# Optimization experiments

Measured on AMD Instinct MI355X. Metric: run time of the kernel, lower is better.

## Reference

```python
import jax, jax.numpy as jnp
import numpy as np

N = 100000   # nodes
E = 1600000  # edges (avg degree 16)
HID = 128    # in_feats = n_hidden
P = 100000   # pos/neg link pairs
L = 3        # GIN layers
BN_EPS = 1e-5


def setup_inputs() -> dict:
    key = jax.random.key(0)
    ks = jax.random.split(key, 16)
    s = 1.0 / np.sqrt(HID)  # ~ torch linear init scale
    inp = {
        "x": jax.random.normal(ks[0], (N, HID), jnp.float32),
        "src": jax.random.randint(ks[1], (E,), 0, N, jnp.int32),
        "dst": jax.random.randint(ks[2], (E,), 0, N, jnp.int32),
        "pos_src": jax.random.randint(ks[3], (P,), 0, N, jnp.int32),
        "pos_dst": jax.random.randint(ks[4], (P,), 0, N, jnp.int32),
        "neg_src": jax.random.randint(ks[5], (P,), 0, N, jnp.int32),
        "neg_dst": jax.random.randint(ks[6], (P,), 0, N, jnp.int32),
        "W0": jax.random.normal(ks[7], (L, HID, HID), jnp.float32) * s,
        "W1": jax.random.normal(ks[8], (L, HID, HID), jnp.float32) * s,
        "g_mlp": jnp.ones((L, HID), jnp.float32),
        "b_mlp": jnp.zeros((L, HID), jnp.float32),
        "g_apply": jnp.ones((L, HID), jnp.float32),
        "b_apply": jnp.zeros((L, HID), jnp.float32),
        "g_out": jnp.ones((L - 1, HID), jnp.float32),
        "b_out": jnp.zeros((L - 1, HID), jnp.float32),
        "pW1": jax.random.normal(ks[9], (HID, HID), jnp.float32) * s,
        "pb1": jnp.zeros((HID,), jnp.float32),
        "pW2": jax.random.normal(ks[10], (HID, HID), jnp.float32) * s,
        "pb2": jnp.zeros((HID,), jnp.float32),
        "pW3": jax.random.normal(ks[11], (1, HID), jnp.float32) * s,
        "pb3": jnp.zeros((1,), jnp.float32),
    }
    return inp


def _bn(h, g, b):
    # training-mode BatchNorm1d: batch stats, biased variance
    mu = jnp.mean(h, axis=0)
    var = jnp.mean(jnp.square(h - mu), axis=0)
    return g * (h - mu) * jax.lax.rsqrt(var + BN_EPS) + b


def reference(x, src, dst, pos_src, pos_dst, neg_src, neg_dst,
              W0, W1, g_mlp, b_mlp, g_apply, b_apply, g_out, b_out,
              pW1, pb1, pW2, pb2, pW3, pb3):
    # in-degree for mean aggregation (clamped to avoid div-by-zero)
    deg = jnp.maximum(
        jax.ops.segment_sum(jnp.ones((E,), x.dtype), dst, num_segments=N), 1.0)
    h = x
    for l in range(L):
        # GINConv, eps = 0: h_dst + mean over in-neighbors
        agg = jax.ops.segment_sum(h[src], dst, num_segments=N) / deg[:, None]
        z = h + agg
        # ApplyNodeFunc: MLP(2 layers, no bias) with inner BN+ReLU, then BN+ReLU
        m = jax.nn.relu(_bn(z @ W0[l].T, g_mlp[l], b_mlp[l]))
        m = m @ W1[l].T
        h = jax.nn.relu(_bn(m, g_apply[l], b_apply[l]))
        if l < L - 1:
            # outer BN + ReLU (dropout is identity in eval)
            h = jax.nn.relu(_bn(h, g_out[l], b_out[l]))

    def predict(hs, hd):
        t = hs * hd
        t = jax.nn.relu(t @ pW1.T + pb1)
        t = jax.nn.relu(t @ pW2.T + pb2)
        return t @ pW3.T + pb3  # [P, 1]

    h_pos = predict(h[pos_src], h[pos_dst])
    h_neg = predict(h[neg_src], h[neg_dst])
    return (h_pos, h_neg)
```

## Files before the change

kernel.cpp:

```cpp
#include <hip/hip_runtime.h>

#define HID 128
#define BN_EPS 1e-5f

typedef __bf16 bf16;
typedef __attribute__((ext_vector_type(8))) __bf16 bf16x8;
typedef __attribute__((ext_vector_type(4))) float f32x4;

__device__ __forceinline__ float bnrelu(float x, float a, float c) {
  return fmaxf(fmaf(a, x, c), 0.f);
}

__global__ void hist_k(const int* __restrict__ dst, int* __restrict__ cnt, int E) {
  int i = blockIdx.x * blockDim.x + threadIdx.x;
  if (i < E) atomicAdd(&cnt[dst[i]], 1);
}

__global__ __launch_bounds__(256)
void scan1_k(const int* __restrict__ cnt, int* __restrict__ bsum, int Nn) {
  __shared__ int red[4];
  int tid = threadIdx.x;
  int base = blockIdx.x * 1024;
  int s = 0;
#pragma unroll
  for (int u = 0; u < 4; ++u) {
    int i = base + u * 256 + tid;
    if (i < Nn) s += cnt[i];
  }
#pragma unroll
  for (int d = 1; d < 64; d <<= 1) s += __shfl_xor(s, d, 64);
  int lane = tid & 63, wv = tid >> 6;
  if (lane == 0) red[wv] = s;
  __syncthreads();
  if (tid == 0) bsum[blockIdx.x] = red[0] + red[1] + red[2] + red[3];
}

__global__ void scan2_k(int* __restrict__ bsum, int G) {
  int lane = threadIdx.x;
  int carry = 0;
  for (int base = 0; base < G; base += 64) {
    int i = base + lane;
    int v = (i < G) ? bsum[i] : 0;
    int x = v;
#pragma unroll
    for (int d = 1; d < 64; d <<= 1) { int t = __shfl_up(x, d, 64); if (lane >= d) x += t; }
    if (i < G) bsum[i] = carry + x - v;
    carry += __shfl(x, 63, 64);
  }
}

__global__ __launch_bounds__(256)
void scan3_k(const int* __restrict__ cnt, const int* __restrict__ boff,
             int* __restrict__ row_start, int Nn, int E) {
  __shared__ int wtot[4];
  int tid = threadIdx.x, lane = tid & 63, wv = tid >> 6;
  int i0 = blockIdx.x * 1024 + tid * 4;
  int t0 = 0, t1 = 0, t2 = 0, t3 = 0;
  if (i0 + 3 < Nn) {
    int4 v = *(const int4*)(cnt + i0);
    t0 = v.x; t1 = v.y; t2 = v.z; t3 = v.w;
  } else {
    if (i0     < Nn) t0 = cnt[i0];
    if (i0 + 1 < Nn) t1 = cnt[i0 + 1];
    if (i0 + 2 < Nn) t2 = cnt[i0 + 2];
    if (i0 + 3 < Nn) t3 = cnt[i0 + 3];
  }
  int tsum = t0 + t1 + t2 + t3;
  int x = tsum;
#pragma unroll
  for (int d = 1; d < 64; d <<= 1) { int t = __shfl_up(x, d, 64); if (lane >= d) x += t; }
  if (lane == 63) wtot[wv] = x;
  __syncthreads();
  int wo = 0;
  for (int k = 0; k < wv; ++k) wo += wtot[k];
  int base = boff[blockIdx.x] + wo + x - tsum;
  if (i0     < Nn) row_start[i0] = base;
  if (i0 + 1 < Nn) row_start[i0 + 1] = base + t0;
  if (i0 + 2 < Nn) row_start[i0 + 2] = base + t0 + t1;
  if (i0 + 3 < Nn) row_start[i0 + 3] = base + t0 + t1 + t2;
  if (blockIdx.x == 0 && tid == 0) row_start[Nn] = E;
}

__global__ void init64_k(const int* __restrict__ row_start, int* __restrict__ bcur64,
                         int Nn, int NB2) {
  int i = threadIdx.x;
  if (i < NB2) {
    int n = i << 11; if (n > Nn) n = Nn;
    bcur64[i] = row_start[n];
  }
}

__global__ __launch_bounds__(256)
void part64_k(const int* __restrict__ src, const int* __restrict__ dst,
              int* __restrict__ bcur64, unsigned* __restrict__ ebuf2, int E) {
  __shared__ int lcnt[64], gbase[64], lcur[64];
  int tid = threadIdx.x;
  if (tid < 64) { lcnt[tid] = 0; lcur[tid] = 0; }
  __syncthreads();
  int base = blockIdx.x * 2048;
  int ok[8]; unsigned pk[8]; int bk[8];
#pragma unroll
  for (int u = 0; u < 8; ++u) {
    int e = base + u * 256 + tid;
    if (e < E) {
      int s = src[e], d = dst[e];
      ok[u] = 1; bk[u] = d >> 11;
      pk[u] = ((unsigned)(d & 2047) << 17) | (unsigned)s;
      atomicAdd(&lcnt[bk[u]], 1);
    } else ok[u] = 0;
  }
  __syncthreads();
  if (tid < 64 && lcnt[tid]) gbase[tid] = atomicAdd(&bcur64[tid], lcnt[tid]);
  __syncthreads();
#pragma unroll
  for (int u = 0; u < 8; ++u) if (ok[u]) {
    int sl = atomicAdd(&lcur[bk[u]], 1);
    ebuf2[gbase[bk[u]] + sl] = pk[u];
  }
}

__global__ __launch_bounds__(1024)
void fill2_k(const unsigned* __restrict__ ebuf2, const int* __restrict__ row_start,
             int* __restrict__ csr, int Nn) {
  __shared__ int ncur[2048];
  int tid = threadIdx.x;
  ncur[tid] = 0; ncur[tid + 1024] = 0;
  __syncthreads();
  int nb0 = blockIdx.x << 11;
  int hi = nb0 + 2048; if (hi > Nn) hi = Nn;
  int beg = row_start[nb0], end = row_start[hi];
  for (int e = beg + tid; e < end; e += 1024) {
    unsigned v = ebuf2[e];
    int dl = v >> 17, s = (int)(v & 0x1FFFF);
    int p = atomicAdd(&ncur[dl], 1);
    csr[row_start[nb0 + dl] + p] = s;
  }
}

__global__ __launch_bounds__(256)
void wconv_k(const float* __restrict__ W0, const float* __restrict__ W1,
             const float* __restrict__ pW1, const float* __restrict__ pW2,
             bf16* __restrict__ Wb) {
  int idx = (blockIdx.x * 256 + threadIdx.x) * 4;
  int seg = idx >> 14, loc = idx & 16383;
  const float* srcp = seg < 3 ? W0 + (size_t)seg * 16384
                    : seg < 6 ? W1 + (size_t)(seg - 3) * 16384
                    : seg == 6 ? pW1 : pW2;
  float4 v = *(const float4*)(srcp + loc);
  union { bf16 h[4]; unsigned long long u; } pk;
  pk.h[0] = (bf16)v.x; pk.h[1] = (bf16)v.y; pk.h[2] = (bf16)v.z; pk.h[3] = (bf16)v.w;
  *(unsigned long long*)(Wb + idx) = pk.u;
}

template<int MODE>
__global__ __launch_bounds__(256)
void agg_k(const float* __restrict__ H,
           const float* __restrict__ ac1, const float* __restrict__ g1, const float* __restrict__ b1,
           const float* __restrict__ ac2, const float* __restrict__ g2, const float* __restrict__ b2,
           float invN,
           const int* __restrict__ row_start, const int* __restrict__ csr,
           bf16* __restrict__ Z, int Nn) {
  __shared__ float sA2[128], sC2[128], sA3[128], sC3[128];
  int tid = threadIdx.x;
  if (MODE) {
    if (tid < 128) {
      float mu = ac1[tid] * invN;
      float var = fmaxf(ac1[128 + tid] * invN - mu * mu, 0.f);
      float a = g1[tid] * rsqrtf(var + BN_EPS);
      sA2[tid] = a; sC2[tid] = fmaf(-a, mu, b1[tid]);
      mu = ac2[tid] * invN;
      var = fmaxf(ac2[128 + tid] * invN - mu * mu, 0.f);
      a = g2[tid] * rsqrtf(var + BN_EPS);
      sA3[tid] = a; sC3[tid] = fmaf(-a, mu, b2[tid]);
    }
    __syncthreads();
  }
  int wv = tid >> 6, lane = tid & 63;
  int n = blockIdx.x * 4 + wv;
  if (n >= Nn) return;
  int c0 = lane * 2;
  float A2x = 0, A2y = 0, C2x = 0, C2y = 0, A3x = 0, A3y = 0, C3x = 0, C3y = 0;
  if (MODE) {
    A2x = sA2[c0]; A2y = sA2[c0 + 1]; C2x = sC2[c0]; C2y = sC2[c0 + 1];
    A3x = sA3[c0]; A3y = sA3[c0 + 1]; C3x = sC3[c0]; C3y = sC3[c0 + 1];
  }
  int beg = row_start[n], end = row_start[n + 1];
  float2 hn = *(const float2*)(H + (size_t)n * HID + c0);
  float inv = 1.f / fmaxf((float)(end - beg), 1.f);
  float ax0 = 0, ay0 = 0, ax1 = 0, ay1 = 0, ax2 = 0, ay2 = 0, ax3 = 0, ay3 = 0;
  int j = beg;
  for (; j + 8 <= end; j += 8) {
    int s0 = csr[j], s1 = csr[j + 1], s2 = csr[j + 2], s3 = csr[j + 3];
    int s4 = csr[j + 4], s5 = csr[j + 5], s6 = csr[j + 6], s7 = csr[j + 7];
    float2 v0 = *(const float2*)(H + (size_t)s0 * HID + c0);
    float2 v1 = *(const float2*)(H + (size_t)s1 * HID + c0);
    float2 v2 = *(const float2*)(H + (size_t)s2 * HID + c0);
    float2 v3 = *(const float2*)(H + (size_t)s3 * HID + c0);
    float2 v4 = *(const float2*)(H + (size_t)s4 * HID + c0);
    float2 v5 = *(const float2*)(H + (size_t)s5 * HID + c0);
    float2 v6 = *(const float2*)(H + (size_t)s6 * HID + c0);
    float2 v7 = *(const float2*)(H + (size_t)s7 * HID + c0);
    if (MODE) {
      v0.x = bnrelu(bnrelu(v0.x, A2x, C2x), A3x, C3x); v0.y = bnrelu(bnrelu(v0.y, A2y, C2y), A3y, C3y);
      v1.x = bnrelu(bnrelu(v1.x, A2x, C2x), A3x, C3x); v1.y = bnrelu(bnrelu(v1.y, A2y, C2y), A3y, C3y);
      v2.x = bnrelu(bnrelu(v2.x, A2x, C2x), A3x, C3x); v2.y = bnrelu(bnrelu(v2.y, A2y, C2y), A3y, C3y);
      v3.x = bnrelu(bnrelu(v3.x, A2x, C2x), A3x, C3x); v3.y = bnrelu(bnrelu(v3.y, A2y, C2y), A3y, C3y);
      v4.x = bnrelu(bnrelu(v4.x, A2x, C2x), A3x, C3x); v4.y = bnrelu(bnrelu(v4.y, A2y, C2y), A3y, C3y);
      v5.x = bnrelu(bnrelu(v5.x, A2x, C2x), A3x, C3x); v5.y = bnrelu(bnrelu(v5.y, A2y, C2y), A3y, C3y);
      v6.x = bnrelu(bnrelu(v6.x, A2x, C2x), A3x, C3x); v6.y = bnrelu(bnrelu(v6.y, A2y, C2y), A3y, C3y);
      v7.x = bnrelu(bnrelu(v7.x, A2x, C2x), A3x, C3x); v7.y = bnrelu(bnrelu(v7.y, A2y, C2y), A3y, C3y);
    }
    ax0 += v0.x; ay0 += v0.y; ax1 += v1.x; ay1 += v1.y;
    ax2 += v2.x; ay2 += v2.y; ax3 += v3.x; ay3 += v3.y;
    ax0 += v4.x; ay0 += v4.y; ax1 += v5.x; ay1 += v5.y;
    ax2 += v6.x; ay2 += v6.y; ax3 += v7.x; ay3 += v7.y;
  }
  for (; j < end; ++j) {
    int s = csr[j];
    float2 v = *(const float2*)(H + (size_t)s * HID + c0);
    if (MODE) {
      v.x = bnrelu(bnrelu(v.x, A2x, C2x), A3x, C3x);
      v.y = bnrelu(bnrelu(v.y, A2y, C2y), A3y, C3y);
    }
    ax0 += v.x; ay0 += v.y;
  }
  float ax = (ax0 + ax1) + (ax2 + ax3);
  float ay = (ay0 + ay1) + (ay2 + ay3);
  float hx = hn.x, hy = hn.y;
  if (MODE) {
    hx = bnrelu(bnrelu(hx, A2x, C2x), A3x, C3x);
    hy = bnrelu(bnrelu(hy, A2y, C2y), A3y, C3y);
  }
  float zx = hx + ax * inv, zy = hy + ay * inv;
  union { bf16 h[2]; unsigned u; } pk;
  pk.h[0] = (bf16)zx; pk.h[1] = (bf16)zy;
  *(unsigned*)((char*)Z + ((size_t)n * HID + c0) * 2) = pk.u;
}

template<int AMODE>
__global__ __launch_bounds__(256)
void gemm_k(const void* __restrict__ Asrc,
            const float* __restrict__ acIn, const float* __restrict__ g, const float* __restrict__ b,
            float invN,
            const bf16* __restrict__ Wb, float* __restrict__ C,
            float* __restrict__ accumOut, int Nrows) {
  __shared__ float sA[128], sC[128], sSum[128], sSq[128];
  int tid = threadIdx.x;
  if (tid < 128) {
    sSum[tid] = 0.f; sSq[tid] = 0.f;
    if (AMODE) {
      float mu = acIn[tid] * invN;
      float var = fmaxf(acIn[128 + tid] * invN - mu * mu, 0.f);
      float a = g[tid] * rsqrtf(var + BN_EPS);
      sA[tid] = a; sC[tid] = fmaf(-a, mu, b[tid]);
    }
  }
  __syncthreads();
  int wv = tid >> 6, lane = tid & 63;
  int lm = lane & 15, lg = lane >> 4;
  int rowbase = blockIdx.x * 128 + wv * 32;
  f32x4 acc[2][8] = {};
#pragma unroll
  for (int kk = 0; kk < 4; ++kk) {
    int kb = kk * 32 + lg * 8;
    bf16x8 af[2];
    if (AMODE == 0) {
      const bf16* Zp = (const bf16*)Asrc;
#pragma unroll
      for (int rt = 0; rt < 2; ++rt) {
        int row = rowbase + rt * 16 + lm; if (row > Nrows - 1) row = Nrows - 1;
        af[rt] = *(const bf16x8*)(Zp + (size_t)row * HID + kb);
      }
    } else {
      const float* Tp = (const float*)Asrc;
      float4 a0 = *(const float4*)(sA + kb), a1 = *(const float4*)(sA + kb + 4);
      float4 q0 = *(const float4*)(sC + kb), q1 = *(const float4*)(sC + kb + 4);
#pragma unroll
      for (int rt = 0; rt < 2; ++rt) {
        int row = rowbase + rt * 16 + lm; if (row > Nrows - 1) row = Nrows - 1;
        const float* p = Tp + (size_t)row * HID + kb;
        float4 x0 = *(const float4*)p, x1 = *(const float4*)(p + 4);
        bf16x8 f;
        f[0] = (bf16)bnrelu(x0.x, a0.x, q0.x); f[1] = (bf16)bnrelu(x0.y, a0.y, q0.y);
        f[2] = (bf16)bnrelu(x0.z, a0.z, q0.z); f[3] = (bf16)bnrelu(x0.w, a0.w, q0.w);
        f[4] = (bf16)bnrelu(x1.x, a1.x, q1.x); f[5] = (bf16)bnrelu(x1.y, a1.y, q1.y);
        f[6] = (bf16)bnrelu(x1.z, a1.z, q1.z); f[7] = (bf16)bnrelu(x1.w, a1.w, q1.w);
        af[rt] = f;
      }
    }
    bf16x8 bfr[8];
#pragma unroll
    for (int ct = 0; ct < 8; ++ct)
      bfr[ct] = *(const bf16x8*)(Wb + (size_t)(ct * 16 + lm) * HID + kb);
#pragma unroll
    for (int rt = 0; rt < 2; ++rt)
#pragma unroll
      for (int ct = 0; ct < 8; ++ct)
        acc[rt][ct] = __builtin_amdgcn_mfma_f32_16x16x32_bf16(af[rt], bfr[ct], acc[rt][ct], 0, 0, 0);
  }
#pragma unroll
  for (int ct = 0; ct < 8; ++ct) {
    int col = ct * 16 + lm;
    float ps = 0.f, pq = 0.f;
#pragma unroll
    for (int rt = 0; rt < 2; ++rt) {
#pragma unroll
      for (int i = 0; i < 4; ++i) {
        int row = rowbase + rt * 16 + lg * 4 + i;
        if (row < Nrows) {
          float v = acc[rt][ct][i];
          C[(size_t)row * HID + col] = v;
          ps += v; pq = fmaf(v, v, pq);
        }
      }
    }
    ps += __shfl_xor(ps, 16, 64); ps += __shfl_xor(ps, 32, 64);
    pq += __shfl_xor(pq, 16, 64); pq += __shfl_xor(pq, 32, 64);
    if (lane < 16) { atomicAdd(&sSum[col], ps); atomicAdd(&sSq[col], pq); }
  }
  __syncthreads();
  if (tid < 128) {
    atomicAdd(&accumOut[tid], sSum[tid]);
    atomicAdd(&accumOut[128 + tid], sSq[tid]);
  }
}

__global__ __launch_bounds__(256)
void stats1_k(const float* __restrict__ T, const float* __restrict__ acIn,
              const float* __restrict__ g, const float* __restrict__ b, float invN,
              float* __restrict__ accumOut, int Nrows) {
  int col = threadIdx.x & 127, half = threadIdx.x >> 7;
  float mu = acIn[col] * invN;
  float var = fmaxf(acIn[128 + col] * invN - mu * mu, 0.f);
  float av = g[col] * rsqrtf(var + BN_EPS);
  float cv = fmaf(-av, mu, b[col]);
  float s = 0.f, sq = 0.f;
  for (int r = blockIdx.x * 2 + half; r < Nrows; r += gridDim.x * 2) {
    float x = T[(size_t)r * HID + col];
    x = fmaxf(fmaf(av, x, cv), 0.f);
    s += x; sq = fmaf(x, x, sq);
  }
  __shared__ float sb[256], qb[256];
  sb[threadIdx.x] = s; qb[threadIdx.x] = sq;
  __syncthreads();
  if (half == 0) {
    s += sb[threadIdx.x + 128]; sq += qb[threadIdx.x + 128];
    atomicAdd(&accumOut[col], s); atomicAdd(&accumOut[128 + col], sq);
  }
}

__global__ __launch_bounds__(256)
void pred_k(const float* __restrict__ T, const float* __restrict__ acIn,
            const float* __restrict__ g, const float* __restrict__ b, float invN,
            const int* __restrict__ ps, const int* __restrict__ pd,
            const int* __restrict__ ns, const int* __restrict__ nd,
            const bf16* __restrict__ W1b, const float* __restrict__ b1p,
            const bf16* __restrict__ W2b, const float* __restrict__ b2p,
            const float* __restrict__ w3, const float* __restrict__ b3,
            float* __restrict__ out, int Pn) {
  __shared__ bf16 At[128 * 128];
  __shared__ float sAp[128], sCp[128];
  int tid = threadIdx.x;
  if (tid < 128) {
    float mu = acIn[tid] * invN;
    float var = fmaxf(acIn[128 + tid] * invN - mu * mu, 0.f);
    float a = g[tid] * rsqrtf(var + BN_EPS);
    sAp[tid] = a; sCp[tid] = fmaf(-a, mu, b[tid]);
  }
  __syncthreads();
  int q0 = blockIdx.x * 128;
  {
    int r = tid >> 1;
    int q = q0 + r;
    int cb = (tid & 1) * 64;
    if (q < 2 * Pn) {
      int s, d;
      if (q < Pn) { s = ps[q]; d = pd[q]; } else { s = ns[q - Pn]; d = nd[q - Pn]; }
      const float* rs_ = T + (size_t)s * HID;
      const float* rd_ = T + (size_t)d * HID;
      for (int c = cb; c < cb + 64; c += 4) {
        float4 xs = *(const float4*)(rs_ + c);
        float4 xd = *(const float4*)(rd_ + c);
        float4 av = *(const float4*)(sAp + c);
        float4 cv = *(const float4*)(sCp + c);
        float t0 = bnrelu(xs.x, av.x, cv.x) * bnrelu(xd.x, av.x, cv.x);
        float t1 = bnrelu(xs.y, av.y, cv.y) * bnrelu(xd.y, av.y, cv.y);
        float t2 = bnrelu(xs.z, av.z, cv.z) * bnrelu(xd.z, av.z, cv.z);
        float t3 = bnrelu(xs.w, av.w, cv.w) * bnrelu(xd.w, av.w, cv.w);
        union { bf16 h[4]; unsigned long long u; } pk;
        pk.h[0] = (bf16)t0; pk.h[1] = (bf16)t1; pk.h[2] = (bf16)t2; pk.h[3] = (bf16)t3;
        unsigned addr = (unsigned)(r * 256 + c * 2);
        addr ^= (unsigned)((r & 7) << 4);
        *(unsigned long long*)((char*)At + addr) = pk.u;
      }
    } else {
      for (int c = cb; c < cb + 64; c += 4) {
        unsigned addr = (unsigned)(r * 256 + c * 2);
        addr ^= (unsigned)((r & 7) << 4);
        *(unsigned long long*)((char*)At + addr) = 0ull;
      }
    }
  }
  __syncthreads();
  int wv = tid >> 6, lane = tid & 63;
  int lm = lane & 15, lg = lane >> 4;
  const f32x4 vzero = {0.f, 0.f, 0.f, 0.f};
  f32x4 acc[2][8];
#pragma unroll
  for (int r = 0; r < 2; ++r) for (int c = 0; c < 8; ++c) acc[r][c] = vzero;
#pragma unroll
  for (int kk = 0; kk < 4; ++kk) {
    bf16x8 af[2];
#pragma unroll
    for (int rt = 0; rt < 2; ++rt) {
      int row = wv * 32 + rt * 16 + lm;
      unsigned addr = (unsigned)(row * 256 + kk * 64 + lg * 16);
      addr ^= (unsigned)((row & 7) << 4);
      af[rt] = *(const bf16x8*)((char*)At + addr);
    }
    bf16x8 bfr[8];
#pragma unroll
    for (int ct = 0; ct < 8; ++ct)
      bfr[ct] = *(const bf16x8*)(W1b + (size_t)(ct * 16 + lm) * HID + kk * 32 + lg * 8);
#pragma unroll
    for (int rt = 0; rt < 2; ++rt)
#pragma unroll
      for (int ct = 0; ct < 8; ++ct)
        acc[rt][ct] = __builtin_amdgcn_mfma_f32_16x16x32_bf16(af[rt], bfr[ct], acc[rt][ct], 0, 0, 0);
  }
  __syncthreads();
#pragma unroll
  for (int rt = 0; rt < 2; ++rt)
#pragma unroll
    for (int ct = 0; ct < 8; ++ct) {
      int col = ct * 16 + lm;
      float bb = b1p[col];
#pragma unroll
      for (int i = 0; i < 4; ++i) {
        int row = wv * 32 + rt * 16 + lg * 4 + i;
        float v = fmaxf(acc[rt][ct][i] + bb, 0.f);
        unsigned addr = (unsigned)(row * 256 + col * 2);
        addr ^= (unsigned)((row & 7) << 4);
        *(bf16*)((char*)At + addr) = (bf16)v;
      }
    }
  __syncthreads();
#pragma unroll
  for (int r = 0; r < 2; ++r) for (int c = 0; c < 8; ++c) acc[r][c] = vzero;
#pragma unroll
  for (int kk = 0; kk < 4; ++kk) {
    bf16x8 af[2];
#pragma unroll
    for (int rt = 0; rt < 2; ++rt) {
      int row = wv * 32 + rt * 16 + lm;
      unsigned addr = (unsigned)(row * 256 + kk * 64 + lg * 16);
      addr ^= (unsigned)((row & 7) << 4);
      af[rt] = *(const bf16x8*)((char*)At + addr);
    }
    bf16x8 bfr[8];
#pragma unroll
    for (int ct = 0; ct < 8; ++ct)
      bfr[ct] = *(const bf16x8*)(W2b + (size_t)(ct * 16 + lm) * HID + kk * 32 + lg * 8);
#pragma unroll
    for (int rt = 0; rt < 2; ++rt)
#pragma unroll
      for (int ct = 0; ct < 8; ++ct)
        acc[rt][ct] = __builtin_amdgcn_mfma_f32_16x16x32_bf16(af[rt], bfr[ct], acc[rt][ct], 0, 0, 0);
  }
  float b2v[8], w3v[8];
#pragma unroll
  for (int ct = 0; ct < 8; ++ct) { b2v[ct] = b2p[ct * 16 + lm]; w3v[ct] = w3[ct * 16 + lm]; }
  float b3s = b3[0];
#pragma unroll
  for (int rt = 0; rt < 2; ++rt) {
#pragma unroll
    for (int i = 0; i < 4; ++i) {
      float p = 0.f;
#pragma unroll
      for (int ct = 0; ct < 8; ++ct)
        p += fmaxf(acc[rt][ct][i] + b2v[ct], 0.f) * w3v[ct];
      p += __shfl_xor(p, 1); p += __shfl_xor(p, 2);
      p += __shfl_xor(p, 4); p += __shfl_xor(p, 8);
      int row = wv * 32 + rt * 16 + lg * 4 + i;
      int q = q0 + row;
      if (lm == 0 && q < 2 * Pn) out[q] = p + b3s;
    }
  }
}

extern "C" void kernel_launch(void* const* d_in, const int* in_sizes, int n_in,
                              void* d_out, int out_size, void* d_ws, size_t ws_size,
                              hipStream_t stream) {
  const float* x  = (const float*)d_in[0];
  const int* src  = (const int*)d_in[1];
  const int* dst  = (const int*)d_in[2];
  const int* ps   = (const int*)d_in[3];
  const int* pd   = (const int*)d_in[4];
  const int* ns   = (const int*)d_in[5];
  const int* nd   = (const int*)d_in[6];
  const float* W0 = (const float*)d_in[7];
  const float* W1 = (const float*)d_in[8];
  const float* g_mlp   = (const float*)d_in[9];
  const float* b_mlp   = (const float*)d_in[10];
  const float* g_apply = (const float*)d_in[11];
  const float* b_apply = (const float*)d_in[12];
  const float* g_out   = (const float*)d_in[13];
  const float* b_out   = (const float*)d_in[14];
  const float* pW1 = (const float*)d_in[15];
  const float* pb1 = (const float*)d_in[16];
  const float* pW2 = (const float*)d_in[17];
  const float* pb2 = (const float*)d_in[18];
  const float* pW3 = (const float*)d_in[19];
  const float* pb3 = (const float*)d_in[20];
  float* out = (float*)d_out;

  const int N = in_sizes[0] / HID;
  const int E = in_sizes[1];
  const int P = in_sizes[3];
  const int NB2 = (N + 2047) >> 11;

  char* w = (char*)d_ws;
  size_t off = 0;
  auto alloc = [&](size_t bytes) -> void* {
    void* p = w + off;
    off = (off + bytes + 255) & ~(size_t)255;
    return p;
  };
  bf16*  Z   = (bf16*)alloc((size_t)N * HID * 2);
  float* TA  = (float*)alloc((size_t)N * HID * 4);
  float* TB  = (float*)alloc((size_t)N * HID * 4);
  int*   csr = (int*)alloc((size_t)E * 4);
  unsigned* ebuf2 = (unsigned*)alloc((size_t)E * 4);
  int*   row_start = (int*)alloc((size_t)(N + 1) * 4);
  size_t zoff = off;
  int*   cnt   = (int*)alloc((size_t)N * 4);
  float* accum = (float*)alloc(9 * 256 * 4);
  size_t zbytes = off - zoff;
  int*   bsum   = (int*)alloc(256 * 4);
  int*   bcur64 = (int*)alloc(64 * 4);
  bf16*  Wb = (bf16*)alloc(8 * 16384 * 2);
  (void)ws_size; (void)n_in; (void)out_size;

  const int G = (N + 1023) / 1024;
  const float invN = 1.f / (float)N;

  hipMemsetAsync(w + zoff, 0, zbytes, stream);
  int gridE = (E + 255) / 256;
  hist_k<<<gridE, 256, 0, stream>>>(dst, cnt, E);
  scan1_k<<<G, 256, 0, stream>>>(cnt, bsum, N);
  scan2_k<<<1, 64, 0, stream>>>(bsum, G);
  scan3_k<<<G, 256, 0, stream>>>(cnt, bsum, row_start, N, E);
  init64_k<<<1, 64, 0, stream>>>(row_start, bcur64, N, NB2);
  part64_k<<<(E + 2047) / 2048, 256, 0, stream>>>(src, dst, bcur64, ebuf2, E);
  fill2_k<<<NB2, 1024, 0, stream>>>(ebuf2, row_start, csr, N);
  wconv_k<<<128, 256, 0, stream>>>(W0, W1, pW1, pW2, Wb);

  int gridN4 = (N + 3) / 4;
  int gridG  = (N + 127) / 128;

  for (int l = 0; l < 3; ++l) {
    int s0 = l * 3 + 0, s1 = l * 3 + 1, s2 = l * 3 + 2;
    if (l == 0)
      agg_k<0><<<gridN4, 256, 0, stream>>>(x, nullptr, nullptr, nullptr,
                                           nullptr, nullptr, nullptr, invN,
                                           row_start, csr, Z, N);
    else {
      int p1 = (l - 1) * 3 + 1, p2 = (l - 1) * 3 + 2;
      agg_k<1><<<gridN4, 256, 0, stream>>>(TB,
                                           accum + p1 * 256, g_apply + (l - 1) * HID, b_apply + (l - 1) * HID,
                                           accum + p2 * 256, g_out + (l - 1) * HID, b_out + (l - 1) * HID,
                                           invN, row_start, csr, Z, N);
    }
    gemm_k<0><<<gridG, 256, 0, stream>>>(Z, nullptr, nullptr, nullptr, invN,
                                         Wb + (size_t)l * 16384, TA, accum + s0 * 256, N);
    gemm_k<1><<<gridG, 256, 0, stream>>>(TA, accum + s0 * 256, g_mlp + l * HID, b_mlp + l * HID, invN,
                                         Wb + (size_t)(3 + l) * 16384, TB, accum + s1 * 256, N);
    if (l < 2)
      stats1_k<<<512, 256, 0, stream>>>(TB, accum + s1 * 256, g_apply + l * HID, b_apply + l * HID,
                                        invN, accum + s2 * 256, N);
  }
  int gridP = (2 * P + 127) / 128;
  pred_k<<<gridP, 256, 0, stream>>>(TB, accum + 7 * 256, g_apply + 2 * HID, b_apply + 2 * HID, invN,
                                    ps, pd, ns, nd,
                                    Wb + (size_t)6 * 16384, pb1,
                                    Wb + (size_t)7 * 16384, pb2,
                                    pW3, pb3, out, P);
}
```

Baseline: 1.048 ms.

## Store intermediate activations in bf16 to halve gather and GEMM traffic

Result: faster. 929.1 us (-11.4%).

```diff
diff --git a/kernel.cpp b/kernel.cpp
--- a/kernel.cpp
+++ b/kernel.cpp
@@ -5,6 +5,7 @@
 
 typedef __bf16 bf16;
 typedef __attribute__((ext_vector_type(8))) __bf16 bf16x8;
+typedef __attribute__((ext_vector_type(2))) __bf16 bf16x2;
 typedef __attribute__((ext_vector_type(4))) float f32x4;
 
 __device__ __forceinline__ float bnrelu(float x, float a, float c) {
@@ -152,26 +153,31 @@
   *(unsigned long long*)(Wb + idx) = pk.u;
 }
 
+__global__ __launch_bounds__(256)
+void xconv_k(const float* __restrict__ X, bf16* __restrict__ Xh, int total) {
+  int idx = (blockIdx.x * 256 + threadIdx.x) * 4;
+  if (idx >= total) return;
+  float4 v = *(const float4*)(X + idx);
+  union { bf16 h[4]; unsigned long long u; } pk;
+  pk.h[0] = (bf16)v.x; pk.h[1] = (bf16)v.y; pk.h[2] = (bf16)v.z; pk.h[3] = (bf16)v.w;
+  *(unsigned long long*)(Xh + idx) = pk.u;
+}
+
 template<int MODE>
 __global__ __launch_bounds__(256)
-void agg_k(const float* __restrict__ H,
-           const float* __restrict__ ac1, const float* __restrict__ g1, const float* __restrict__ b1,
-           const float* __restrict__ ac2, const float* __restrict__ g2, const float* __restrict__ b2,
+void agg_k(const bf16* __restrict__ Hh,
+           const float* __restrict__ ac, const float* __restrict__ g, const float* __restrict__ b,
            float invN,
            const int* __restrict__ row_start, const int* __restrict__ csr,
            bf16* __restrict__ Z, int Nn) {
-  __shared__ float sA2[128], sC2[128], sA3[128], sC3[128];
+  __shared__ float sA[128], sC[128];
   int tid = threadIdx.x;
   if (MODE) {
     if (tid < 128) {
-      float mu = ac1[tid] * invN;
-      float var = fmaxf(ac1[128 + tid] * invN - mu * mu, 0.f);
-      float a = g1[tid] * rsqrtf(var + BN_EPS);
-      sA2[tid] = a; sC2[tid] = fmaf(-a, mu, b1[tid]);
-      mu = ac2[tid] * invN;
-      var = fmaxf(ac2[128 + tid] * invN - mu * mu, 0.f);
-      a = g2[tid] * rsqrtf(var + BN_EPS);
-      sA3[tid] = a; sC3[tid] = fmaf(-a, mu, b2[tid]);
+      float mu = ac[tid] * invN;
+      float var = fmaxf(ac[128 + tid] * invN - mu * mu, 0.f);
+      float a = g[tid] * rsqrtf(var + BN_EPS);
+      sA[tid] = a; sC[tid] = fmaf(-a, mu, b[tid]);
     }
     __syncthreads();
   }
@@ -179,70 +185,66 @@
   int n = blockIdx.x * 4 + wv;
   if (n >= Nn) return;
   int c0 = lane * 2;
-  float A2x = 0, A2y = 0, C2x = 0, C2y = 0, A3x = 0, A3y = 0, C3x = 0, C3y = 0;
-  if (MODE) {
-    A2x = sA2[c0]; A2y = sA2[c0 + 1]; C2x = sC2[c0]; C2y = sC2[c0 + 1];
-    A3x = sA3[c0]; A3y = sA3[c0 + 1]; C3x = sC3[c0]; C3y = sC3[c0 + 1];
-  }
+  float Ax = 0, Ay = 0, Cx = 0, Cy = 0;
+  if (MODE) { Ax = sA[c0]; Ay = sA[c0 + 1]; Cx = sC[c0]; Cy = sC[c0 + 1]; }
   int beg = row_start[n], end = row_start[n + 1];
-  float2 hn = *(const float2*)(H + (size_t)n * HID + c0);
+  bf16x2 hn = *(const bf16x2*)(Hh + (size_t)n * HID + c0);
   float inv = 1.f / fmaxf((float)(end - beg), 1.f);
   float ax0 = 0, ay0 = 0, ax1 = 0, ay1 = 0, ax2 = 0, ay2 = 0, ax3 = 0, ay3 = 0;
   int j = beg;
   for (; j + 8 <= end; j += 8) {
     int s0 = csr[j], s1 = csr[j + 1], s2 = csr[j + 2], s3 = csr[j + 3];
     int s4 = csr[j + 4], s5 = csr[j + 5], s6 = csr[j + 6], s7 = csr[j + 7];
-    float2 v0 = *(const float2*)(H + (size_t)s0 * HID + c0);
-    float2 v1 = *(const float2*)(H + (size_t)s1 * HID + c0);
-    float2 v2 = *(const float2*)(H + (size_t)s2 * HID + c0);
-    float2 v3 = *(const float2*)(H + (size_t)s3 * HID + c0);
-    float2 v4 = *(const float2*)(H + (size_t)s4 * HID + c0);
-    float2 v5 = *(const float2*)(H + (size_t)s5 * HID + c0);
-    float2 v6 = *(const float2*)(H + (size_t)s6 * HID + c0);
-    float2 v7 = *(const float2*)(H + (size_t)s7 * HID + c0);
+    bf16x2 v0 = *(const bf16x2*)(Hh + (size_t)s0 * HID + c0);
+    bf16x2 v1 = *(const bf16x2*)(Hh + (size_t)s1 * HID + c0);
+    bf16x2 v2 = *(const bf16x2*)(Hh + (size_t)s2 * HID + c0);
+    bf16x2 v3 = *(const bf16x2*)(Hh + (size_t)s3 * HID + c0);
+    bf16x2 v4 = *(const bf16x2*)(Hh + (size_t)s4 * HID + c0);
+    bf16x2 v5 = *(const bf16x2*)(Hh + (size_t)s5 * HID + c0);
+    bf16x2 v6 = *(const bf16x2*)(Hh + (size_t)s6 * HID + c0);
+    bf16x2 v7 = *(const bf16x2*)(Hh + (size_t)s7 * HID + c0);
+    float x0 = (float)v0[0], y0 = (float)v0[1], x1 = (float)v1[0], y1 = (float)v1[1];
+    float x2 = (float)v2[0], y2 = (float)v2[1], x3 = (float)v3[0], y3 = (float)v3[1];
+    float x4 = (float)v4[0], y4 = (float)v4[1], x5 = (float)v5[0], y5 = (float)v5[1];
+    float x6 = (float)v6[0], y6 = (float)v6[1], x7 = (float)v7[0], y7 = (float)v7[1];
     if (MODE) {
-      v0.x = bnrelu(bnrelu(v0.x, A2x, C2x), A3x, C3x); v0.y = bnrelu(bnrelu(v0.y, A2y, C2y), A3y, C3y);
-      v1.x = bnrelu(bnrelu(v1.x, A2x, C2x), A3x, C3x); v1.y = bnrelu(bnrelu(v1.y, A2y, C2y), A3y, C3y);
-      v2.x = bnrelu(bnrelu(v2.x, A2x, C2x), A3x, C3x); v2.y = bnrelu(bnrelu(v2.y, A2y, C2y), A3y, C3y);
-      v3.x = bnrelu(bnrelu(v3.x, A2x, C2x), A3x, C3x); v3.y = bnrelu(bnrelu(v3.y, A2y, C2y), A3y, C3y);
-      v4.x = bnrelu(bnrelu(v4.x, A2x, C2x), A3x, C3x); v4.y = bnrelu(bnrelu(v4.y, A2y, C2y), A3y, C3y);
-      v5.x = bnrelu(bnrelu(v5.x, A2x, C2x), A3x, C3x); v5.y = bnrelu(bnrelu(v5.y, A2y, C2y), A3y, C3y);
-      v6.x = bnrelu(bnrelu(v6.x, A2x, C2x), A3x, C3x); v6.y = bnrelu(bnrelu(v6.y, A2y, C2y), A3y, C3y);
-      v7.x = bnrelu(bnrelu(v7.x, A2x, C2x), A3x, C3x); v7.y = bnrelu(bnrelu(v7.y, A2y, C2y), A3y, C3y);
-    }
-    ax0 += v0.x; ay0 += v0.y; ax1 += v1.x; ay1 += v1.y;
-    ax2 += v2.x; ay2 += v2.y; ax3 += v3.x; ay3 += v3.y;
-    ax0 += v4.x; ay0 += v4.y; ax1 += v5.x; ay1 += v5.y;
-    ax2 += v6.x; ay2 += v6.y; ax3 += v7.x; ay3 += v7.y;
+      x0 = bnrelu(x0, Ax, Cx); y0 = bnrelu(y0, Ay, Cy);
+      x1 = bnrelu(x1, Ax, Cx); y1 = bnrelu(y1, Ay, Cy);
+      x2 = bnrelu(x2, Ax, Cx); y2 = bnrelu(y2, Ay, Cy);
+      x3 = bnrelu(x3, Ax, Cx); y3 = bnrelu(y3, Ay, Cy);
+      x4 = bnrelu(x4, Ax, Cx); y4 = bnrelu(y4, Ay, Cy);
+      x5 = bnrelu(x5, Ax, Cx); y5 = bnrelu(y5, Ay, Cy);
+      x6 = bnrelu(x6, Ax, Cx); y6 = bnrelu(y6, Ay, Cy);
+      x7 = bnrelu(x7, Ax, Cx); y7 = bnrelu(y7, Ay, Cy);
+    }
+    ax0 += x0; ay0 += y0; ax1 += x1; ay1 += y1;
+    ax2 += x2; ay2 += y2; ax3 += x3; ay3 += y3;
+    ax0 += x4; ay0 += y4; ax1 += x5; ay1 += y5;
+    ax2 += x6; ay2 += y6; ax3 += x7; ay3 += y7;
   }
   for (; j < end; ++j) {
     int s = csr[j];
-    float2 v = *(const float2*)(H + (size_t)s * HID + c0);
-    if (MODE) {
-      v.x = bnrelu(bnrelu(v.x, A2x, C2x), A3x, C3x);
-      v.y = bnrelu(bnrelu(v.y, A2y, C2y), A3y, C3y);
-    }
-    ax0 += v.x; ay0 += v.y;
+    bf16x2 v = *(const bf16x2*)(Hh + (size_t)s * HID + c0);
+    float vx = (float)v[0], vy = (float)v[1];
+    if (MODE) { vx = bnrelu(vx, Ax, Cx); vy = bnrelu(vy, Ay, Cy); }
+    ax0 += vx; ay0 += vy;
   }
   float ax = (ax0 + ax1) + (ax2 + ax3);
   float ay = (ay0 + ay1) + (ay2 + ay3);
-  float hx = hn.x, hy = hn.y;
-  if (MODE) {
-    hx = bnrelu(bnrelu(hx, A2x, C2x), A3x, C3x);
-    hy = bnrelu(bnrelu(hy, A2y, C2y), A3y, C3y);
-  }
+  float hx = (float)hn[0], hy = (float)hn[1];
+  if (MODE) { hx = bnrelu(hx, Ax, Cx); hy = bnrelu(hy, Ay, Cy); }
   float zx = hx + ax * inv, zy = hy + ay * inv;
   union { bf16 h[2]; unsigned u; } pk;
   pk.h[0] = (bf16)zx; pk.h[1] = (bf16)zy;
   *(unsigned*)((char*)Z + ((size_t)n * HID + c0) * 2) = pk.u;
 }
 
-template<int AMODE>
-__global__ __launch_bounds__(256)
-void gemm_k(const void* __restrict__ Asrc,
+template<int AMODE, int OUTF>
+__global__ __launch_bounds__(256)
+void gemm_k(const bf16* __restrict__ Asrc,
             const float* __restrict__ acIn, const float* __restrict__ g, const float* __restrict__ b,
             float invN,
-            const bf16* __restrict__ Wb, float* __restrict__ C,
+            const bf16* __restrict__ Wb, bf16* __restrict__ Cb, float* __restrict__ Cf,
             float* __restrict__ accumOut, int Nrows) {
   __shared__ float sA[128], sC[128], sSum[128], sSq[128];
   int tid = threadIdx.x;
@@ -264,27 +266,20 @@
   for (int kk = 0; kk < 4; ++kk) {
     int kb = kk * 32 + lg * 8;
     bf16x8 af[2];
-    if (AMODE == 0) {
-      const bf16* Zp = (const bf16*)Asrc;
-#pragma unroll
-      for (int rt = 0; rt < 2; ++rt) {
-        int row = rowbase + rt * 16 + lm; if (row > Nrows - 1) row = Nrows - 1;
-        af[rt] = *(const bf16x8*)(Zp + (size_t)row * HID + kb);
-      }
-    } else {
-      const float* Tp = (const float*)Asrc;
-      float4 a0 = *(const float4*)(sA + kb), a1 = *(const float4*)(sA + kb + 4);
-      float4 q0 = *(const float4*)(sC + kb), q1 = *(const float4*)(sC + kb + 4);
-#pragma unroll
-      for (int rt = 0; rt < 2; ++rt) {
-        int row = rowbase + rt * 16 + lm; if (row > Nrows - 1) row = Nrows - 1;
-        const float* p = Tp + (size_t)row * HID + kb;
-        float4 x0 = *(const float4*)p, x1 = *(const float4*)(p + 4);
+#pragma unroll
+    for (int rt = 0; rt < 2; ++rt) {
+      int row = rowbase + rt * 16 + lm; if (row > Nrows - 1) row = Nrows - 1;
+      bf16x8 raw = *(const bf16x8*)(Asrc + (size_t)row * HID + kb);
+      if (AMODE == 0) {
+        af[rt] = raw;
+      } else {
+        float4 a0 = *(const float4*)(sA + kb), a1 = *(const float4*)(sA + kb + 4);
+        float4 q0 = *(const float4*)(sC + kb), q1 = *(const float4*)(sC + kb + 4);
         bf16x8 f;
-        f[0] = (bf16)bnrelu(x0.x, a0.x, q0.x); f[1] = (bf16)bnrelu(x0.y, a0.y, q0.y);
-        f[2] = (bf16)bnrelu(x0.z, a0.z, q0.z); f[3] = (bf16)bnrelu(x0.w, a0.w, q0.w);
-        f[4] = (bf16)bnrelu(x1.x, a1.x, q1.x); f[5] = (bf16)bnrelu(x1.y, a1.y, q1.y);
-        f[6] = (bf16)bnrelu(x1.z, a1.z, q1.z); f[7] = (bf16)bnrelu(x1.w, a1.w, q1.w);
+        f[0] = (bf16)bnrelu((float)raw[0], a0.x, q0.x); f[1] = (bf16)bnrelu((float)raw[1], a0.y, q0.y);
+        f[2] = (bf16)bnrelu((float)raw[2], a0.z, q0.z); f[3] = (bf16)bnrelu((float)raw[3], a0.w, q0.w);
+        f[4] = (bf16)bnrelu((float)raw[4], a1.x, q1.x); f[5] = (bf16)bnrelu((float)raw[5], a1.y, q1.y);
+        f[6] = (bf16)bnrelu((float)raw[6], a1.z, q1.z); f[7] = (bf16)bnrelu((float)raw[7], a1.w, q1.w);
         af[rt] = f;
       }
     }
@@ -309,7 +304,8 @@
         int row = rowbase + rt * 16 + lg * 4 + i;
         if (row < Nrows) {
           float v = acc[rt][ct][i];
-          C[(size_t)row * HID + col] = v;
+          if (OUTF) Cf[(size_t)row * HID + col] = v;
+          else      Cb[(size_t)row * HID + col] = (bf16)v;
           ps += v; pq = fmaf(v, v, pq);
         }
       }
@@ -328,7 +324,7 @@
 __global__ __launch_bounds__(256)
 void stats1_k(const float* __restrict__ T, const float* __restrict__ acIn,
               const float* __restrict__ g, const float* __restrict__ b, float invN,
-              float* __restrict__ accumOut, int Nrows) {
+              float* __restrict__ accumOut, bf16* __restrict__ Y, int Nrows) {
   int col = threadIdx.x & 127, half = threadIdx.x >> 7;
   float mu = acIn[col] * invN;
   float var = fmaxf(acIn[128 + col] * invN - mu * mu, 0.f);
@@ -338,6 +334,7 @@
   for (int r = blockIdx.x * 2 + half; r < Nrows; r += gridDim.x * 2) {
     float x = T[(size_t)r * HID + col];
     x = fmaxf(fmaf(av, x, cv), 0.f);
+    Y[(size_t)r * HID + col] = (bf16)x;
     s += x; sq = fmaf(x, x, sq);
   }
   __shared__ float sb[256], qb[256];
@@ -527,8 +524,10 @@
     return p;
   };
   bf16*  Z   = (bf16*)alloc((size_t)N * HID * 2);
-  float* TA  = (float*)alloc((size_t)N * HID * 4);
+  bf16*  TAb = (bf16*)alloc((size_t)N * HID * 2);
   float* TB  = (float*)alloc((size_t)N * HID * 4);
+  bf16*  Yb  = (bf16*)alloc((size_t)N * HID * 2);
+  bf16*  Xh  = (bf16*)alloc((size_t)N * HID * 2);
   int*   csr = (int*)alloc((size_t)E * 4);
   unsigned* ebuf2 = (unsigned*)alloc((size_t)E * 4);
   int*   row_start = (int*)alloc((size_t)(N + 1) * 4);
@@ -554,6 +553,7 @@
   part64_k<<<(E + 2047) / 2048, 256, 0, stream>>>(src, dst, bcur64, ebuf2, E);
   fill2_k<<<NB2, 1024, 0, stream>>>(ebuf2, row_start, csr, N);
   wconv_k<<<128, 256, 0, stream>>>(W0, W1, pW1, pW2, Wb);
+  xconv_k<<<(N * HID / 4 + 255) / 256, 256, 0, stream>>>(x, Xh, N * HID);
 
   int gridN4 = (N + 3) / 4;
   int gridG  = (N + 127) / 128;
@@ -561,23 +561,23 @@
   for (int l = 0; l < 3; ++l) {
     int s0 = l * 3 + 0, s1 = l * 3 + 1, s2 = l * 3 + 2;
     if (l == 0)
-      agg_k<0><<<gridN4, 256, 0, stream>>>(x, nullptr, nullptr, nullptr,
-                                           nullptr, nullptr, nullptr, invN,
+      agg_k<0><<<gridN4, 256, 0, stream>>>(Xh, nullptr, nullptr, nullptr, invN,
                                            row_start, csr, Z, N);
     else {
-      int p1 = (l - 1) * 3 + 1, p2 = (l - 1) * 3 + 2;
-      agg_k<1><<<gridN4, 256, 0, stream>>>(TB,
-                                           accum + p1 * 256, g_apply + (l - 1) * HID, b_apply + (l - 1) * HID,
+      int p2 = (l - 1) * 3 + 2;
+      agg_k<1><<<gridN4, 256, 0, stream>>>(Yb,
                                            accum + p2 * 256, g_out + (l - 1) * HID, b_out + (l - 1) * HID,
                                            invN, row_start, csr, Z, N);
     }
-    gemm_k<0><<<gridG, 256, 0, stream>>>(Z, nullptr, nullptr, nullptr, invN,
-                                         Wb + (size_t)l * 16384, TA, accum + s0 * 256, N);
-    gemm_k<1><<<gridG, 256, 0, stream>>>(TA, accum + s0 * 256, g_mlp + l * HID, b_mlp + l * HID, invN,
-                                         Wb + (size_t)(3 + l) * 16384, TB, accum + s1 * 256, N);
+    gemm_k<0, 0><<<gridG, 256, 0, stream>>>(Z, nullptr, nullptr, nullptr, invN,
+                                            Wb + (size_t)l * 16384, TAb, nullptr,
+                                            accum + s0 * 256, N);
+    gemm_k<1, 1><<<gridG, 256, 0, stream>>>(TAb, accum + s0 * 256, g_mlp + l * HID, b_mlp + l * HID,
+                                            invN, Wb + (size_t)(3 + l) * 16384, nullptr, TB,
+                                            accum + s1 * 256, N);
     if (l < 2)
       stats1_k<<<512, 256, 0, stream>>>(TB, accum + s1 * 256, g_apply + l * HID, b_apply + l * HID,
-                                        invN, accum + s2 * 256, N);
+                                        invN, accum + s2 * 256, Yb, N);
   }
   int gridP = (2 * P + 127) / 128;
   pred_k<<<gridP, 256, 0, stream>>>(TB, accum + 7 * 256, g_apply + 2 * HID, b_apply + 2 * HID, invN,
```
